# Kernel tuning notes

Hardware: AMD Instinct MI355X
Metric: run time of the kernel (lower is better)

Reference implementation:

```python
import jax, jax.numpy as jnp
import numpy as np

N_BOXES = 2048
N_CLASSES = 20


def _cross(a, b):
    return a[..., 0] * b[..., 1] - a[..., 1] * b[..., 0]


def _corners(box):
    # box: [5] = cx, cy, w, h, angle -> [4,2] corner coords
    cx, cy, w, h, a = box[0], box[1], box[2], box[3], box[4]
    c, s = jnp.cos(a), jnp.sin(a)
    dx = jnp.array([-1.0, 1.0, 1.0, -1.0], box.dtype) * (w * 0.5)
    dy = jnp.array([-1.0, -1.0, 1.0, 1.0], box.dtype) * (h * 0.5)
    return jnp.stack([cx + c * dx - s * dy, cy + s * dx + c * dy], axis=-1)


def _points_in_box(pts, box):
    # pts [K,2]; rotate into box frame, test axis-aligned containment
    cx, cy, w, h, a = box[0], box[1], box[2], box[3], box[4]
    c, s = jnp.cos(a), jnp.sin(a)
    px = pts[:, 0] - cx
    py = pts[:, 1] - cy
    lx = c * px + s * py
    ly = -s * px + c * py
    eps = 1e-5
    return (jnp.abs(lx) <= w * 0.5 + eps) & (jnp.abs(ly) <= h * 0.5 + eps)


def _pair_inter_area(box_a, box_b):
    # Exact convex intersection area of two rotated rectangles.
    ca = _corners(box_a)
    cb = _corners(box_b)
    # all 4x4 edge-pair intersections
    p = ca[:, None, :]
    r = (jnp.roll(ca, -1, 0) - ca)[:, None, :]
    q = cb[None, :, :]
    s_ = (jnp.roll(cb, -1, 0) - cb)[None, :, :]
    denom = _cross(r, s_)
    qp = q - p
    safe = jnp.where(jnp.abs(denom) > 1e-9, denom, 1.0)
    t = _cross(qp, s_) / safe
    u = _cross(qp, r) / safe
    valid_e = (jnp.abs(denom) > 1e-9) & (t >= 0.0) & (t <= 1.0) & (u >= 0.0) & (u <= 1.0)
    ipts = p + t[..., None] * r  # [4,4,2]
    # candidate polygon vertices: corners of A in B, corners of B in A, edge crossings
    pts = jnp.concatenate([ca, cb, ipts.reshape(16, 2)], axis=0)  # [24,2]
    mask = jnp.concatenate([_points_in_box(ca, box_b), _points_in_box(cb, box_a), valid_e.reshape(16)], axis=0)
    k = jnp.sum(mask)
    m = mask.astype(pts.dtype)[:, None]
    center = jnp.sum(pts * m, axis=0) / jnp.maximum(k, 1).astype(pts.dtype)
    d = pts - center
    ang = jnp.where(mask, jnp.arctan2(d[:, 1], d[:, 0]), 1e9)  # invalid -> sorted last
    idx = jnp.argsort(ang)
    ds = d[idx]
    ar = jnp.arange(24)
    nxt = jnp.where(ar + 1 < k, ar + 1, 0)
    cr = _cross(ds, ds[nxt])
    area = 0.5 * jnp.abs(jnp.sum(jnp.where(ar < k, cr, 0.0)))
    return jnp.where(k >= 3, area, 0.0)


def _iou_one_vs_many(box, boxes):
    inter = jax.vmap(lambda b: _pair_inter_area(box, b))(boxes)  # [N]
    area_a = box[2] * box[3]
    area_b = boxes[:, 2] * boxes[:, 3]
    return inter / (area_a + area_b - inter + 1e-9)


def _rotated_nms_mask(boxes, scores, iou_threshold):
    # sequential greedy suppression, highest score first; returns bool keep mask (original order)
    n = boxes.shape[0]
    order = jnp.argsort(-scores)
    bs = boxes[order]
    ar = jnp.arange(n)

    def body(i, keep):
        ious = _iou_one_vs_many(bs[i], bs)
        suppress = (ious > iou_threshold) & (ar > i) & keep[i]
        return keep & ~suppress

    keep_sorted = jax.lax.fori_loop(0, n, body, jnp.ones((n,), bool))
    return jnp.zeros((n,), bool).at[order].set(keep_sorted)


def setup_inputs() -> dict:
    key = jax.random.key(0)
    k1, k2, k3, k4, k5 = jax.random.split(key, 5)
    cxcy = jax.random.uniform(k1, (N_BOXES, 2), jnp.float32) * 1024.0
    wh = jax.random.uniform(k2, (N_BOXES, 2), jnp.float32) * 96.0 + 4.0
    ang = jax.random.uniform(k3, (N_BOXES, 1), jnp.float32) * np.pi
    boxes = jnp.concatenate([cxcy, wh, ang], axis=1)  # [N,5]
    scores = jax.random.uniform(k4, (N_BOXES,), jnp.float32)
    labels = jax.random.randint(k5, (N_BOXES,), 0, N_CLASSES, dtype=jnp.int64 if jax.config.read('jax_enable_x64') else jnp.int32)
    return {"boxes": boxes, "scores": scores, "labels": labels, "iou_threshold": 0.5}


def reference(boxes, scores, labels, iou_threshold):
    # multiclass NMS via coordinate-offset trick (N <= 20000 branch of forward)
    cx, cy, w, h = boxes[:, 0], boxes[:, 1], boxes[:, 2], boxes[:, 3]
    max_radius = jnp.max(jnp.sqrt(w * w + h * h)) * 0.5
    max_coord = jnp.maximum(jnp.max(cx), jnp.max(cy))
    offset_scale = (max_coord + max_radius) * 2.0 + 1.0
    offsets = labels.astype(boxes.dtype) * offset_scale
    boxes_nms = boxes.at[:, 0].add(offsets).at[:, 1].add(offsets)
    keep = _rotated_nms_mask(boxes_nms, scores, iou_threshold)
    # fixed-shape encoding of the kept-index set: score of kept boxes, 0 for suppressed
    return scores * keep.astype(scores.dtype)
```

## Files before the change

kernel.cpp:

```cpp
#include <hip/hip_runtime.h>
#include <cstdint>

typedef unsigned long long u64;
typedef uint32_t u32;

#define NB 2048
#define EDGE_CAP 16384
#define EDGE_LDS 16384
#define CLIST_CAP 2048


__device__ __forceinline__ bool pt_in(float px, float py, float cx, float cy,
                                      float hw, float hh, float c, float s) {
#pragma clang fp contract(off)
  float ax = px - cx;
  float ay = py - cy;
  float lx = c * ax + s * ay;
  float ly = c * ay - s * ax;
  return (fabsf(lx) <= hw + 1e-5f) && (fabsf(ly) <= hh + 1e-5f);
}

__device__ float pair_inter_area(float acx, float acy, float aw, float ah,
                                 float ac, float as_, float bcx, float bcy,
                                 float bw, float bh, float bc, float bs_) {
#pragma clang fp contract(off)
  const float SX[4] = {-1.f, 1.f, 1.f, -1.f};
  const float SY[4] = {-1.f, -1.f, 1.f, 1.f};
  float axx[4], ayy[4], bxx[4], byy[4];
  float ahw = aw * 0.5f, ahh = ah * 0.5f;
  float bhw = bw * 0.5f, bhh = bh * 0.5f;
#pragma unroll
  for (int q = 0; q < 4; ++q) {
    float dx = SX[q] * ahw, dy = SY[q] * ahh;
    axx[q] = acx + ac * dx - as_ * dy;
    ayy[q] = acy + as_ * dx + ac * dy;
    float ex = SX[q] * bhw, ey = SY[q] * bhh;
    bxx[q] = bcx + bc * ex - bs_ * ey;
    byy[q] = bcy + bs_ * ex + bc * ey;
  }
  float px_[24], py_[24];
  bool mk[24];
#pragma unroll
  for (int q = 0; q < 4; ++q) {
    px_[q] = axx[q]; py_[q] = ayy[q];
    mk[q] = pt_in(axx[q], ayy[q], bcx, bcy, bhw, bhh, bc, bs_);
    px_[4 + q] = bxx[q]; py_[4 + q] = byy[q];
    mk[4 + q] = pt_in(bxx[q], byy[q], acx, acy, ahw, ahh, ac, as_);
  }
#pragma unroll
  for (int e = 0; e < 4; ++e) {
    float rx = axx[(e + 1) & 3] - axx[e];
    float ry = ayy[(e + 1) & 3] - ayy[e];
#pragma unroll
    for (int f = 0; f < 4; ++f) {
      float sx = bxx[(f + 1) & 3] - bxx[f];
      float sy = byy[(f + 1) & 3] - byy[f];
      float denom = rx * sy - ry * sx;
      float qpx = bxx[f] - axx[e];
      float qpy = byy[f] - ayy[e];
      bool dn = fabsf(denom) > 1e-9f;
      float safe = dn ? denom : 1.0f;
      float t = (qpx * sy - qpy * sx) / safe;
      float uu = (qpx * ry - qpy * rx) / safe;
      bool valid = dn && (t >= 0.0f) && (t <= 1.0f) && (uu >= 0.0f) && (uu <= 1.0f);
      int id = 8 + e * 4 + f;
      px_[id] = axx[e] + t * rx;
      py_[id] = ayy[e] + t * ry;
      mk[id] = valid;
    }
  }
  int k = 0;
  float sx0 = 0.0f, sy0 = 0.0f;
#pragma unroll
  for (int q = 0; q < 24; ++q) {
    if (mk[q]) { k++; sx0 += px_[q]; sy0 += py_[q]; }
  }
  float kk = (float)(k > 0 ? k : 1);
  float cxm = sx0 / kk, cym = sy0 / kk;
  u64 key[32];
  float dxr[32], dyr[32];
#pragma unroll
  for (int q = 0; q < 24; ++q) {
    float dx = px_[q] - cxm, dy = py_[q] - cym;
    dxr[q] = dx; dyr[q] = dy;
    float ang = mk[q] ? atan2f(dy, dx) : 1e9f;
    u32 ub = __float_as_uint(ang);
    u32 v = (ub & 0x80000000u) ? ~ub : (ub | 0x80000000u);
    key[q] = (((u64)v) << 5) | (u64)q;
  }
#pragma unroll
  for (int q = 24; q < 32; ++q) { key[q] = ~0ull; dxr[q] = 0.f; dyr[q] = 0.f; }
#pragma unroll
  for (int kk2 = 2; kk2 <= 32; kk2 <<= 1) {
#pragma unroll
    for (int jj = kk2 >> 1; jj > 0; jj >>= 1) {
#pragma unroll
      for (int ii = 0; ii < 32; ++ii) {
        int ll = ii ^ jj;
        if (ll > ii) {
          bool up = ((ii & kk2) == 0);
          u64 ka = key[ii], kb = key[ll];
          bool sw = up ? (ka > kb) : (ka < kb);
          key[ii] = sw ? kb : ka;
          key[ll] = sw ? ka : kb;
          float da = dxr[ii], db = dxr[ll];
          dxr[ii] = sw ? db : da;
          dxr[ll] = sw ? da : db;
          float ea = dyr[ii], eb = dyr[ll];
          dyr[ii] = sw ? eb : ea;
          dyr[ll] = sw ? ea : eb;
        }
      }
    }
  }
  float acc = 0.0f;
#pragma unroll
  for (int q = 0; q < 24; ++q) {
    if (q < k - 1) {
      acc += dxr[q] * dyr[q + 1] - dyr[q] * dxr[q + 1];
    } else if (q == k - 1) {
      acc += dxr[q] * dyr[0] - dyr[q] * dxr[0];
    }
  }
  float area = 0.5f * fabsf(acc);
  return (k >= 3) ? area : 0.0f;
}

__global__ __launch_bounds__(256) void build_kernel(
    const float* __restrict__ boxes, const float* __restrict__ scores,
    const int* __restrict__ labels,
    float* __restrict__ cxp, float* __restrict__ cyp, float* __restrict__ wp,
    float* __restrict__ hp, float* __restrict__ cp, float* __restrict__ sp,
    float* __restrict__ radp, float* __restrict__ sscp, int* __restrict__ sidx,
    u32* __restrict__ counters) {
#pragma clang fp contract(off)
  __shared__ float sc[NB];
  __shared__ float smc[4], smr[4];
  int t = threadIdx.x;
  if (blockIdx.x == 0 && t < 2) counters[t] = 0u;
  float mc = -1e30f, mr = -1e30f;
  for (int k = t; k < NB; k += 256) {
    float cx = boxes[k * 5 + 0];
    float cy = boxes[k * 5 + 1];
    float w = boxes[k * 5 + 2];
    float h = boxes[k * 5 + 3];
    mc = fmaxf(mc, fmaxf(cx, cy));
    float ww = w * w;
    float hh = h * h;
    mr = fmaxf(mr, sqrtf(ww + hh));
    sc[k] = scores[k];
  }
  for (int off = 32; off > 0; off >>= 1) {
    mc = fmaxf(mc, __shfl_down(mc, off));
    mr = fmaxf(mr, __shfl_down(mr, off));
  }
  if ((t & 63) == 0) { smc[t >> 6] = mc; smr[t >> 6] = mr; }
  __syncthreads();
  mc = fmaxf(fmaxf(smc[0], smc[1]), fmaxf(smc[2], smc[3]));
  mr = fmaxf(fmaxf(smr[0], smr[1]), fmaxf(smr[2], smr[3]));
  float osc = (mc + mr * 0.5f) * 2.0f + 1.0f;

  int wave = t >> 6, lane = t & 63;
  int i = blockIdx.x * 4 + wave;
  float si = sc[i];
  int rank = 0;
#pragma unroll 8
  for (int m = 0; m < NB / 64; ++m) {
    int j = m * 64 + lane;
    float sj = sc[j];
    rank += (int)((sj > si) || (sj == si && j < i));
  }
  for (int off = 32; off > 0; off >>= 1) rank += __shfl_down(rank, off);
  if (lane == 0) {
    float off = (float)labels[i] * osc;
    float cx = boxes[i * 5 + 0] + off;
    float cy = boxes[i * 5 + 1] + off;
    float w = boxes[i * 5 + 2];
    float h = boxes[i * 5 + 3];
    float a = boxes[i * 5 + 4];
    float c = cosf(a);
    float s = sinf(a);
    float ww = w * w;
    float hh = h * h;
    cxp[rank] = cx;
    cyp[rank] = cy;
    wp[rank] = w;
    hp[rank] = h;
    cp[rank] = c;
    sp[rank] = s;
    radp[rank] = 0.5f * sqrtf(ww + hh);
    sscp[rank] = si;
    sidx[rank] = i;
  }
}

__global__ __launch_bounds__(256) void candgeom_kernel(
    const float* __restrict__ cxp, const float* __restrict__ cyp,
    const float* __restrict__ wp, const float* __restrict__ hp,
    const float* __restrict__ cp, const float* __restrict__ sp,
    const float* __restrict__ radp, const float* __restrict__ thrp,
    u32* __restrict__ edges, u32* __restrict__ counters) {
#pragma clang fp contract(off)
  __shared__ float lx[NB], ly[NB], lr[NB];
  __shared__ u32 clist[CLIST_CAP];
  __shared__ u32 ccnt;
  int t = threadIdx.x;
  if (t == 0) ccnt = 0;
  for (int k = t; k < NB; k += 256) {
    lx[k] = cxp[k];
    ly[k] = cyp[k];
    lr[k] = radp[k];
  }
  __syncthreads();
  int i0 = blockIdx.x * 8;
#pragma unroll
  for (int di = 0; di < 8; ++di) {
    int i = i0 + di;
    float ax = lx[i], ay = ly[i], ar = lr[i];
#pragma unroll
    for (int c = 0; c < 8; ++c) {
      int j = c * 256 + t;
      if (j > i) {
        float dx = lx[j] - ax, dy = ly[j] - ay;
        float rr = ar + lr[j] + 1.0f;
        if (dx * dx + dy * dy <= rr * rr) {
          u32 s = atomicAdd(&ccnt, 1u);
          if (s < CLIST_CAP) clist[s] = ((u32)i << 16) | (u32)j;
        }
      }
    }
  }
  __syncthreads();
  u32 cnt = ccnt < CLIST_CAP ? ccnt : CLIST_CAP;
  float thr = *thrp;
  for (u32 idx = t; idx < cnt; idx += 256) {
    u32 pk = clist[idx];
    int i = (int)(pk >> 16);
    int j = (int)(pk & 0xFFFFu);
    float acx = cxp[i], acy = cyp[i], aw = wp[i], ah = hp[i];
    float ac = cp[i], as_ = sp[i];
    float bcx = cxp[j], bcy = cyp[j], bw = wp[j], bh = hp[j];
    float bc = cp[j], bs_ = sp[j];
    float inter = pair_inter_area(acx, acy, aw, ah, ac, as_,
                                  bcx, bcy, bw, bh, bc, bs_);
    float areaA = aw * ah;
    float areaB = bw * bh;
    float iou = inter / (areaA + areaB - inter + 1e-9f);
    if (iou > thr) {
      u32 e = atomicAdd(&counters[1], 1u);
      if (e < EDGE_CAP) edges[e] = pk;
    }
  }
}

__global__ __launch_bounds__(256) void greedy_out_kernel(
    const u32* __restrict__ edges, const u32* __restrict__ counters,
    const float* __restrict__ sscp, const int* __restrict__ sidx,
    float* __restrict__ out) {
  __shared__ u64 keepw[32];
  __shared__ u32 Sw32[64];
  __shared__ int changed;
  __shared__ u32 eL[EDGE_LDS];
  int t = threadIdx.x;
  u32 ecnt = counters[1];
  if (ecnt > EDGE_CAP) ecnt = EDGE_CAP;
  u32 nl = ecnt < EDGE_LDS ? ecnt : EDGE_LDS;
  for (u32 k = t; k < nl; k += 256) eL[k] = edges[k];
  if (t < 32) keepw[t] = ~0ull;
  __syncthreads();
  for (int iter = 0; iter < 2060; ++iter) {
    if (t < 64) Sw32[t] = 0u;
    if (t == 0) changed = 0;
    __syncthreads();
    for (u32 k = t; k < ecnt; k += 256) {
      u32 pk = (k < EDGE_LDS) ? eL[k] : edges[k];
      int i = (int)(pk >> 16);
      int j = (int)(pk & 0xFFFFu);
      if ((keepw[i >> 6] >> (i & 63)) & 1ull)
        atomicOr(&Sw32[j >> 5], 1u << (j & 31));
    }
    __syncthreads();
    if (t < 32) {
      u64 S = ((u64)Sw32[2 * t]) | (((u64)Sw32[2 * t + 1]) << 32);
      u64 nk = ~S;
      if (nk != keepw[t]) { keepw[t] = nk; changed = 1; }
    }
    __syncthreads();
    int ch = changed;
    __syncthreads();
    if (!ch) break;
  }
  for (int p = t; p < NB; p += 256) {
    int bit = (int)((keepw[p >> 6] >> (p & 63)) & 1ull);
    out[sidx[p]] = bit ? sscp[p] : 0.0f;
  }
}

extern "C" void kernel_launch(void* const* d_in, const int* in_sizes, int n_in,
                              void* d_out, int out_size, void* d_ws, size_t ws_size,
                              hipStream_t stream) {
  const float* boxes = (const float*)d_in[0];
  const float* scores = (const float*)d_in[1];
  const int* labels = (const int*)d_in[2];
  const float* thr = (const float*)d_in[3];
  float* out = (float*)d_out;

  char* base = (char*)d_ws;
  u32* counters = (u32*)base;
  float* arr = (float*)(base + 256);
  float* cxp = arr + 0 * NB;
  float* cyp = arr + 1 * NB;
  float* wp = arr + 2 * NB;
  float* hp = arr + 3 * NB;
  float* cp = arr + 4 * NB;
  float* sp = arr + 5 * NB;
  float* radp = arr + 6 * NB;
  float* sscp = arr + 7 * NB;
  int* sidx = (int*)(base + 66048);
  u32* edges = (u32*)(base + 81920);

  build_kernel<<<512, 256, 0, stream>>>(boxes, scores, labels, cxp, cyp, wp, hp,
                                        cp, sp, radp, sscp, sidx, counters);
  candgeom_kernel<<<256, 256, 0, stream>>>(cxp, cyp, wp, hp, cp, sp, radp,
                                           thr, edges, counters);
  greedy_out_kernel<<<1, 256, 0, stream>>>(edges, counters, sscp, sidx, out);
}
```

Before: 89.98 us.

## Fuse greedy suppression into candidate kernel via last-block-done pattern

Merges the single-block greedy NMS kernel into the candidate/IoU kernel. An atomic completion counter picks the last finishing block, which then runs the iterative keep-mask fixpoint and writes the output, saving one kernel launch. The edge cache in LDS is cut to reuse the existing 2048-entry clist buffer, so edges beyond that are read from global memory on every iteration. The fixpoint also now runs in a block with higher LDS use.

```diff
diff --git a/kernel.cpp b/kernel.cpp
--- a/kernel.cpp
+++ b/kernel.cpp
@@ -6,7 +6,6 @@
 
 #define NB 2048
 #define EDGE_CAP 16384
-#define EDGE_LDS 16384
 #define CLIST_CAP 2048
 
 
@@ -137,7 +136,7 @@
   __shared__ float sc[NB];
   __shared__ float smc[4], smr[4];
   int t = threadIdx.x;
-  if (blockIdx.x == 0 && t < 2) counters[t] = 0u;
+  if (blockIdx.x == 0 && t < 4) counters[t] = 0u;
   float mc = -1e30f, mr = -1e30f;
   for (int k = t; k < NB; k += 256) {
     float cx = boxes[k * 5 + 0];
@@ -194,16 +193,22 @@
   }
 }
 
-__global__ __launch_bounds__(256) void candgeom_kernel(
+__global__ __launch_bounds__(256) void candgeom_greedy_kernel(
     const float* __restrict__ cxp, const float* __restrict__ cyp,
     const float* __restrict__ wp, const float* __restrict__ hp,
     const float* __restrict__ cp, const float* __restrict__ sp,
     const float* __restrict__ radp, const float* __restrict__ thrp,
-    u32* __restrict__ edges, u32* __restrict__ counters) {
+    const float* __restrict__ sscp, const int* __restrict__ sidx,
+    u32* __restrict__ edges, u32* __restrict__ counters,
+    float* __restrict__ out) {
 #pragma clang fp contract(off)
   __shared__ float lx[NB], ly[NB], lr[NB];
   __shared__ u32 clist[CLIST_CAP];
   __shared__ u32 ccnt;
+  __shared__ int is_last;
+  __shared__ u64 keepw[32];
+  __shared__ u32 Sw32[64];
+  __shared__ int changed;
   int t = threadIdx.x;
   if (t == 0) ccnt = 0;
   for (int k = t; k < NB; k += 256) {
@@ -251,21 +256,20 @@
       if (e < EDGE_CAP) edges[e] = pk;
     }
   }
-}
-
-__global__ __launch_bounds__(256) void greedy_out_kernel(
-    const u32* __restrict__ edges, const u32* __restrict__ counters,
-    const float* __restrict__ sscp, const int* __restrict__ sidx,
-    float* __restrict__ out) {
-  __shared__ u64 keepw[32];
-  __shared__ u32 Sw32[64];
-  __shared__ int changed;
-  __shared__ u32 eL[EDGE_LDS];
-  int t = threadIdx.x;
+  __syncthreads();
+  if (t == 0) {
+    __threadfence();
+    u32 old = atomicAdd(&counters[2], 1u);
+    is_last = (old == (u32)(gridDim.x - 1)) ? 1 : 0;
+  }
+  __syncthreads();
+  if (!is_last) return;
+  __threadfence();
+  __syncthreads();
   u32 ecnt = counters[1];
   if (ecnt > EDGE_CAP) ecnt = EDGE_CAP;
-  u32 nl = ecnt < EDGE_LDS ? ecnt : EDGE_LDS;
-  for (u32 k = t; k < nl; k += 256) eL[k] = edges[k];
+  u32 nl = ecnt < CLIST_CAP ? ecnt : CLIST_CAP;
+  for (u32 k = t; k < nl; k += 256) clist[k] = edges[k];
   if (t < 32) keepw[t] = ~0ull;
   __syncthreads();
   for (int iter = 0; iter < 2060; ++iter) {
@@ -273,7 +277,7 @@
     if (t == 0) changed = 0;
     __syncthreads();
     for (u32 k = t; k < ecnt; k += 256) {
-      u32 pk = (k < EDGE_LDS) ? eL[k] : edges[k];
+      u32 pk = (k < CLIST_CAP) ? clist[k] : edges[k];
       int i = (int)(pk >> 16);
       int j = (int)(pk & 0xFFFFu);
       if ((keepw[i >> 6] >> (i & 63)) & 1ull)
@@ -321,7 +325,7 @@
 
   build_kernel<<<512, 256, 0, stream>>>(boxes, scores, labels, cxp, cyp, wp, hp,
                                         cp, sp, radp, sscp, sidx, counters);
-  candgeom_kernel<<<256, 256, 0, stream>>>(cxp, cyp, wp, hp, cp, sp, radp,
-                                           thr, edges, counters);
-  greedy_out_kernel<<<1, 256, 0, stream>>>(edges, counters, sscp, sidx, out);
-}
+  candgeom_greedy_kernel<<<256, 256, 0, stream>>>(cxp, cyp, wp, hp, cp, sp,
+                                                  radp, thr, sscp, sidx,
+                                                  edges, counters, out);
+}
```

After: 91.46 us. No clear change (+1.6%).
